# Performance work log

Hardware: AMD Instinct MI355X
Metric: run time of the kernel (lower is better)

The kernel has to match this reference:

```python
import jax, jax.numpy as jnp
import numpy as np

N, H, E, ED = 50000, 128, 600000, 32
LN_EPS = 1e-5


def _mlp(x, W1, b1, W2, b2):
    h = jax.nn.gelu(x @ W1 + b1, approximate=False)
    return h @ W2 + b2


def setup_inputs() -> dict:
    key = jax.random.key(0)
    ks = jax.random.split(key, 12)
    s = lambda fan_in: 1.0 / np.sqrt(fan_in)
    return {
        "x": jax.random.normal(ks[0], (N, H), dtype=jnp.float32),
        "edge_index": jax.random.randint(ks[1], (2, E), 0, N, dtype=jnp.int64),
        "edge_attr": jax.random.normal(ks[2], (E, ED), dtype=jnp.float32),
        "eW1": jax.random.normal(ks[3], (2 * H + ED, H), dtype=jnp.float32) * s(2 * H + ED),
        "eb1": jnp.zeros((H,), dtype=jnp.float32),
        "eW2": jax.random.normal(ks[4], (H, H), dtype=jnp.float32) * s(H),
        "eb2": jnp.zeros((H,), dtype=jnp.float32),
        "nW1": jax.random.normal(ks[5], (2 * H, H), dtype=jnp.float32) * s(2 * H),
        "nb1": jnp.zeros((H,), dtype=jnp.float32),
        "nW2": jax.random.normal(ks[6], (H, H), dtype=jnp.float32) * s(H),
        "nb2": jnp.zeros((H,), dtype=jnp.float32),
        "ln_g": jnp.ones((H,), dtype=jnp.float32),
        "ln_b": jnp.zeros((H,), dtype=jnp.float32),
    }


def reference(x, edge_index, edge_attr, eW1, eb1, eW2, eb2, nW1, nb1, nW2, nb2, ln_g, ln_b):
    src, dst = edge_index[0], edge_index[1]
    # edge MLP on gathered endpoint features + edge attrs: [E, 2H+ED] -> [E, H]
    msg = _mlp(jnp.concatenate([x[src], x[dst], edge_attr], axis=-1), eW1, eb1, eW2, eb2)
    # scatter-mean into destination nodes
    agg = jax.ops.segment_sum(msg, dst, num_segments=x.shape[0])
    count = jax.ops.segment_sum(jnp.ones((dst.shape[0], 1), dtype=x.dtype), dst, num_segments=x.shape[0])
    agg = agg / (count + 1e-8)
    # node MLP + residual + layernorm
    out = _mlp(jnp.concatenate([x, agg], axis=-1), nW1, nb1, nW2, nb2) + x
    mu = jnp.mean(out, axis=-1, keepdims=True)
    var = jnp.mean(jnp.square(out - mu), axis=-1, keepdims=True)
    return (out - mu) * jax.lax.rsqrt(var + LN_EPS) * ln_g + ln_b
```

## Files before the change

### kernel.cpp

```cpp
#include <hip/hip_runtime.h>
#include <hip/hip_fp16.h>
#include <math.h>

#define NN 50000
#define HH 128
#define EE 600000
#define EDD 32
#define NBINS 50176
#define NPRE 782

typedef __attribute__((ext_vector_type(8))) _Float16 half8;
typedef __attribute__((ext_vector_type(4))) float f32x4;

__device__ __forceinline__ unsigned pkh(float a, float b) {
  __half2 h = __floats2half2_rn(a, b);
  return *reinterpret_cast<unsigned*>(&h);
}
__device__ __forceinline__ unsigned hadd2u(unsigned a, unsigned b) {
  __half2 x = *reinterpret_cast<__half2*>(&a);
  __half2 y = *reinterpret_cast<__half2*>(&b);
  __half2 s = __hadd2(x, y);
  return *reinterpret_cast<unsigned*>(&s);
}
__device__ __forceinline__ float lo16f(unsigned u) {
  __half2 h = *reinterpret_cast<__half2*>(&u);
  return __low2float(h);
}
__device__ __forceinline__ float hi16f(unsigned u) {
  __half2 h = *reinterpret_cast<__half2*>(&u);
  return __high2float(h);
}
__device__ __forceinline__ short f2hs(float f) {
  __half h = __float2half_rn(f);
  return *reinterpret_cast<short*>(&h);
}
__device__ __forceinline__ float h2f(short s) {
  __half h = *reinterpret_cast<__half*>(&s);
  return __half2float(h);
}

__device__ __forceinline__ float gelu_f(float v) {
  float u = 2.3022082f * v * fmaf(0.044715f, v * v, 1.0f);
  float e = __builtin_amdgcn_exp2f(u);
  float r = __builtin_amdgcn_rcpf(e + 1.0f);
  return fmaf(-v, r, v);
}

#define FS 132
__global__ __launch_bounds__(256) void k_setup(
    const float* __restrict__ eW1, const float* __restrict__ nW1,
    const float* __restrict__ nW2, const float* __restrict__ eW2,
    const float* __restrict__ eb2, const long long* __restrict__ ei,
    long long nmax,
    short* __restrict__ pe1, short* __restrict__ pn1, short* __restrict__ pn2,
    short* __restrict__ pnW2p, float* __restrict__ b2p,
    int* __restrict__ zbase, int* __restrict__ flag) {
  __shared__ short sA[64 * 136];
  __shared__ float sR[64 * FS];
  __shared__ int bad;
  const int blk = blockIdx.x;
  const int tid = threadIdx.x;

  if (blk < 42) {
    const int b = blk * 4 + (tid >> 6);
    const int l = tid & 63;
    const float* W;
    short* P;
    int bb;
    if (b < 72)       { W = eW1; P = pe1; bb = b; }
    else if (b < 136) { W = nW1; P = pn1; bb = b - 72; }
    else              { W = nW2; P = pn2; bb = b - 136; }
    const int kt = bb >> 3, ct = bb & 7;
    short v[8];
#pragma unroll
    for (int j = 0; j < 8; ++j)
      v[j] = f2hs(W[(size_t)(kt * 32 + ((l >> 4) * 8 + j)) * HH + ct * 16 + (l & 15)]);
    short* dst = P + ((size_t)bb * 64 + l) * 8;
#pragma unroll
    for (int j = 0; j < 8; ++j) dst[j] = v[j];
    return;
  }
  if (blk == 42) {
    if (tid == 0) bad = 0;
    __syncthreads();
    for (int i = tid; i < 2048; i += 256) {
      long long v = ei[i];
      if (v < 0 || v >= nmax) bad = 1;
    }
    __syncthreads();
    if (tid == 0) *flag = (bad ? 0 : 1);
    return;
  }
  if (blk < 92) {
    int idx = (blk - 43) * 2048 + tid * 8;
    int4 z = {0, 0, 0, 0};
    *(int4*)(zbase + idx) = z;
    *(int4*)(zbase + idx + 4) = z;
    return;
  }
  if (blk == 94) {
    if (tid < 128) {
      float acc = 0.f;
#pragma unroll 4
      for (int k = 0; k < 128; ++k)
        acc += eb2[k] * nW1[(size_t)(128 + k) * HH + tid];
      b2p[tid] = acc;
    }
    return;
  }
  {
    const int b = blk - 92;
    const int le = tid >> 2, lq = tid & 3;
    const int wv = tid >> 6, l = tid & 63, lr = l & 15, kq = l >> 4;

    half8 bf[8];
#pragma unroll
    for (int kt = 0; kt < 4; ++kt)
#pragma unroll
      for (int c = 0; c < 2; ++c) {
        half8 v;
#pragma unroll
        for (int j = 0; j < 8; ++j)
          v[j] = (_Float16)nW1[(size_t)(128 + kt * 32 + ((l >> 4) * 8 + j)) * HH +
                               (wv * 2 + c) * 16 + (l & 15)];
        bf[kt * 2 + c] = v;
      }
    {
      const float4* xs = (const float4*)(eW2 + (size_t)(64 * b + le) * HH);
#pragma unroll
      for (int i = 0; i < 4; ++i) {
        float4 a = xs[lq * 8 + i * 2], c = xs[lq * 8 + i * 2 + 1];
        uint4 u = {pkh(a.x, a.y), pkh(a.z, a.w), pkh(c.x, c.y), pkh(c.z, c.w)};
        *(uint4*)&sA[le * 136 + lq * 32 + i * 8] = u;
      }
    }
    __syncthreads();

    f32x4 acc[4][2];
    const f32x4 zero = {0.f, 0.f, 0.f, 0.f};
#pragma unroll
    for (int m = 0; m < 4; ++m) { acc[m][0] = zero; acc[m][1] = zero; }
    const short* ab = &sA[lr * 136 + kq * 8];
#pragma unroll
    for (int kt = 0; kt < 4; ++kt) {
      half8 af[4];
#pragma unroll
      for (int m = 0; m < 4; ++m) af[m] = *(const half8*)(ab + m * 16 * 136 + kt * 32);
#pragma unroll
      for (int m = 0; m < 4; ++m)
#pragma unroll
        for (int c = 0; c < 2; ++c)
          acc[m][c] = __builtin_amdgcn_mfma_f32_16x16x32_f16(af[m], bf[kt * 2 + c], acc[m][c], 0, 0, 0);
    }
#pragma unroll
    for (int c = 0; c < 2; ++c)
#pragma unroll
      for (int m = 0; m < 4; ++m)
#pragma unroll
        for (int r = 0; r < 4; ++r)
          sR[(m * 16 + kq * 4 + r) * FS + wv * 32 + c * 16 + lr] = acc[m][c][r];
    __syncthreads();

#pragma unroll
    for (int it = 0; it < 4; ++it) {
      int item = tid + 256 * it;
      int lane = item & 63;
      int pair = item >> 6;
      int ktl = pair >> 3, ct = pair & 7;
      short v[8];
#pragma unroll
      for (int j = 0; j < 8; ++j) {
        int rowl = ktl * 32 + ((lane >> 4) * 8 + j);
        int colp = ct * 16 + (lane & 15);
        v[j] = f2hs(sR[rowl * FS + colp]);
      }
      short* dst = pnW2p + (((size_t)(2 * b + ktl) * 8 + ct) * 64 + lane) * 8;
#pragma unroll
      for (int j = 0; j < 8; ++j) dst[j] = v[j];
    }
  }
}

__global__ __launch_bounds__(256, 4) void k_preh(
    const float* __restrict__ x, const short* __restrict__ pW1,
    const void* __restrict__ eiv, const int* __restrict__ flag,
    unsigned* __restrict__ Psw, unsigned* __restrict__ Pdw,
    float* __restrict__ Hagg, int* __restrict__ chist) {
  __shared__ short sX[64 * 136];
  const int blk = blockIdx.x;
  const int tid = threadIdx.x;

  if (blk >= NPRE) {
    int e = (blk - NPRE) * 256 + tid;
    if (e < EE) {
      int d;
      if (*flag) d = (int)((const long long*)eiv)[EE + e];
      else       d = ((const int*)eiv)[EE + e];
      atomicAdd(&chist[d], 1);
    }
    return;
  }

  const int r0 = blk * 64;
  const int le = tid >> 2, lq = tid & 3;
  const int wv = tid >> 6, l = tid & 63, lr = l & 15, kq = l >> 4;

  {
    int gr = r0 + le;
    if (gr < NN) {
      float4 z = {0.f, 0.f, 0.f, 0.f};
      float4* hp = (float4*)(Hagg + (size_t)gr * HH) + lq * 8;
#pragma unroll
      for (int i = 0; i < 8; ++i) hp[i] = z;
    }
  }

  const half8* bp = (const half8*)pW1;
  half8 fa[8], fb[8];
#pragma unroll
  for (int kt = 0; kt < 4; ++kt)
#pragma unroll
    for (int c = 0; c < 2; ++c) {
      fa[kt * 2 + c] = bp[(kt * 8 + wv * 2 + c) * 64 + l];
      fb[kt * 2 + c] = bp[((kt + 4) * 8 + wv * 2 + c) * 64 + l];
    }
  {
    int gr = r0 + le;
    if (gr < NN) {
      const float4* xs = (const float4*)(x + (size_t)gr * HH);
#pragma unroll
      for (int i = 0; i < 4; ++i) {
        float4 a = xs[lq * 8 + i * 2], c = xs[lq * 8 + i * 2 + 1];
        uint4 u = {pkh(a.x, a.y), pkh(a.z, a.w), pkh(c.x, c.y), pkh(c.z, c.w)};
        *(uint4*)&sX[le * 136 + lq * 32 + i * 8] = u;
      }
    } else {
      uint4 z = {0, 0, 0, 0};
#pragma unroll
      for (int i = 0; i < 4; ++i) *(uint4*)&sX[le * 136 + lq * 32 + i * 8] = z;
    }
  }
  __syncthreads();

  f32x4 as_[4][2], ad[4][2];
  const f32x4 zero = {0.f, 0.f, 0.f, 0.f};
#pragma unroll
  for (int m = 0; m < 4; ++m) { as_[m][0] = zero; as_[m][1] = zero; ad[m][0] = zero; ad[m][1] = zero; }
  const short* ab = &sX[lr * 136 + kq * 8];
#pragma unroll
  for (int kt = 0; kt < 4; ++kt) {
    half8 af[4];
#pragma unroll
    for (int m = 0; m < 4; ++m) af[m] = *(const half8*)(ab + m * 16 * 136 + kt * 32);
#pragma unroll
    for (int m = 0; m < 4; ++m)
#pragma unroll
      for (int c = 0; c < 2; ++c) {
        as_[m][c] = __builtin_amdgcn_mfma_f32_16x16x32_f16(af[m], fa[kt * 2 + c], as_[m][c], 0, 0, 0);
        ad[m][c] = __builtin_amdgcn_mfma_f32_16x16x32_f16(af[m], fb[kt * 2 + c], ad[m][c], 0, 0, 0);
      }
  }
#pragma unroll
  for (int m = 0; m < 4; ++m)
#pragma unroll
    for (int r = 0; r < 4; ++r) {
      int grow = r0 + m * 16 + kq * 4 + r;
      if (grow < NN) {
        Psw[(size_t)grow * 64 + wv * 16 + lr] = pkh(as_[m][0][r], as_[m][1][r]);
        Pdw[(size_t)grow * 64 + wv * 16 + lr] = pkh(ad[m][0][r], ad[m][1][r]);
      }
    }
}

__global__ void k_scan1(const int* __restrict__ chist, int* __restrict__ tmp,
                        int* __restrict__ bsum) {
  __shared__ int buf[2][256];
  int t = threadIdx.x;
  int i = blockIdx.x * 256 + t;
  buf[0][t] = chist[i];
  __syncthreads();
  int cur = 0;
  for (int o = 1; o < 256; o <<= 1) {
    int v = buf[cur][t];
    if (t >= o) v += buf[cur][t - o];
    buf[cur ^ 1][t] = v;
    __syncthreads();
    cur ^= 1;
  }
  tmp[i] = buf[cur][t];
  if (t == 255) bsum[blockIdx.x] = buf[cur][255];
}

__global__ void k_scan2(int* __restrict__ bsum) {
  __shared__ int buf[2][256];
  int t = threadIdx.x;
  int orig = (t < 196) ? bsum[t] : 0;
  buf[0][t] = orig;
  __syncthreads();
  int cur = 0;
  for (int o = 1; o < 256; o <<= 1) {
    int v = buf[cur][t];
    if (t >= o) v += buf[cur][t - o];
    buf[cur ^ 1][t] = v;
    __syncthreads();
    cur ^= 1;
  }
  if (t < 196) bsum[t] = buf[cur][t] - orig;
}

__global__ void k_scatter(const void* __restrict__ eiv, const int* __restrict__ flag,
                          const int* __restrict__ tmp, const int* __restrict__ chist,
                          const int* __restrict__ bsum, int* __restrict__ cntW,
                          int4* __restrict__ e4) {
  int e = blockIdx.x * blockDim.x + threadIdx.x;
  if (e >= EE) return;
  int s, d;
  if (*flag) {
    const long long* p = (const long long*)eiv;
    s = (int)p[e];
    d = (int)p[EE + e];
  } else {
    const int* p = (const int*)eiv;
    s = p[e];
    d = p[EE + e];
  }
  int base = tmp[d] - chist[d] + bsum[d >> 8];
  int pos = base + atomicAdd(&cntW[d], 1);
  e4[pos] = make_int4(s, d, e, 0);
}

#define SFP 68
__global__ __launch_bounds__(256, 7) void k_edge(
    const unsigned* __restrict__ Psw, const unsigned* __restrict__ Pdw,
    const float* __restrict__ ea,
    const short* __restrict__ pW1, const float* __restrict__ b1,
    const int4* __restrict__ e4, float* __restrict__ Hagg) {
  __shared__ unsigned sFp[64 * SFP];
  __shared__ short sEA[64 * 40];
  __shared__ int sDst[64];

  const int tid = threadIdx.x;
  const int e0 = blockIdx.x * 64;
  const int le = tid >> 2, lq = tid & 3;
  const int wv = tid >> 6, l = tid & 63, lr = l & 15, kq = l >> 4;

  half8 w1c[2];
#pragma unroll
  for (int c = 0; c < 2; ++c)
    w1c[c] = ((const half8*)pW1)[(64 + wv * 2 + c) * 64 + l];

  const int4 er = e4[e0 + le];
  if (lq == 0) sDst[le] = er.y;

  {
    const uint4* ps = (const uint4*)(Psw + (size_t)er.x * 64);
    const uint4* pd = (const uint4*)(Pdw + (size_t)er.y * 64);
#pragma unroll
    for (int i = 0; i < 4; ++i) {
      uint4 a = ps[lq * 4 + i];
      uint4 b = pd[lq * 4 + i];
      uint4 s = {hadd2u(a.x, b.x), hadd2u(a.y, b.y), hadd2u(a.z, b.z), hadd2u(a.w, b.w)};
      *(uint4*)&sFp[le * SFP + lq * 16 + i * 4] = s;
    }
    const float4* ep = (const float4*)(ea + (size_t)er.z * EDD);
    float4 a = ep[lq * 2], b = ep[lq * 2 + 1];
    uint4 u = {pkh(a.x, a.y), pkh(a.z, a.w), pkh(b.x, b.y), pkh(b.z, b.w)};
    *(uint4*)&sEA[le * 40 + lq * 8] = u;
  }
  __syncthreads();

  f32x4 acc[4][2];
  const f32x4 zero = {0.f, 0.f, 0.f, 0.f};
#pragma unroll
  for (int m = 0; m < 4; ++m) { acc[m][0] = zero; acc[m][1] = zero; }
  {
#pragma unroll
    for (int m = 0; m < 4; ++m) {
      half8 af = *(const half8*)&sEA[(m * 16 + lr) * 40 + kq * 8];
#pragma unroll
      for (int c = 0; c < 2; ++c)
        acc[m][c] = __builtin_amdgcn_mfma_f32_16x16x32_f16(af, w1c[c], acc[m][c], 0, 0, 0);
    }
  }

  const float b1c0 = b1[wv * 32 + lr];
  const float b1c1 = b1[wv * 32 + 16 + lr];
#pragma unroll
  for (int m = 0; m < 4; ++m)
#pragma unroll
    for (int r = 0; r < 4; ++r) {
      const int row = m * 16 + kq * 4 + r;
      unsigned up = sFp[row * SFP + wv * 16 + lr];
      float v0 = acc[m][0][r] + lo16f(up) + b1c0;
      float v1 = acc[m][1][r] + hi16f(up) + b1c1;
      sFp[row * SFP + wv * 16 + lr] = pkh(gelu_f(v0), gelu_f(v1));
    }
  __syncthreads();

  {
    const int p = tid & 63;
    const int q = tid >> 6;
    const int c0 = (p >> 4) * 32 + (p & 15);
    const int rend = q * 16 + 15;
    float r0s = 0.f, r1s = 0.f;
#pragma unroll 4
    for (int r = q * 16; r <= rend; ++r) {
      unsigned u = sFp[r * SFP + p];
      r0s += lo16f(u);
      r1s += hi16f(u);
      int dcur = sDst[r];
      bool last = (r == rend) || (sDst[r + 1] != dcur);
      if (last) {
        atomicAdd(&Hagg[(size_t)dcur * HH + c0], r0s);
        atomicAdd(&Hagg[(size_t)dcur * HH + c0 + 16], r1s);
        r0s = 0.f;
        r1s = 0.f;
      }
    }
  }
}

#define NS 264
__global__ __launch_bounds__(256, 4) void k_node(
    const float* __restrict__ x,
    const float* __restrict__ Hagg, const int* __restrict__ chist,
    const short* __restrict__ pn1, const short* __restrict__ pnW2p,
    const float* __restrict__ nb1, const float* __restrict__ b2p,
    const short* __restrict__ pn2, const float* __restrict__ nb2,
    const float* __restrict__ g, const float* __restrict__ be,
    float* __restrict__ out) {
  __shared__ short sA[64 * NS];
  __shared__ float sP[64 * 4];
  __shared__ float sP2[64 * 4];
  __shared__ float sFac[64];

  const int tid = threadIdx.x;
  const int r0 = blockIdx.x * 64;
  const int le = tid >> 2;
  const int lq = tid & 3;
  const int wv = tid >> 6;
  const int l = tid & 63;
  const int lr = l & 15;
  const int kq = l >> 4;

  const half8* bpa = (const half8*)pn1;
  const half8* bpc = (const half8*)pnW2p;
  half8 b1f[16];
#pragma unroll
  for (int kt = 0; kt < 4; ++kt)
#pragma unroll
    for (int c = 0; c < 2; ++c) {
      b1f[kt * 2 + c] = bpa[(kt * 8 + wv * 2 + c) * 64 + l];
      b1f[(kt + 4) * 2 + c] = bpc[(kt * 8 + wv * 2 + c) * 64 + l];
    }

  {
    const int gr = r0 + le;
    short* row = &sA[le * NS];
    if (gr < NN) {
      float cntf = (float)chist[gr];
      float rinv = 1.0f / (cntf + 1e-8f);
      if (lq == 0) sFac[le] = cntf * rinv;
      const float4* xs = (const float4*)(x + (size_t)gr * HH);
#pragma unroll
      for (int i = 0; i < 4; ++i) {
        float4 a = xs[lq * 8 + i * 2], c = xs[lq * 8 + i * 2 + 1];
        uint4 u = {pkh(a.x, a.y), pkh(a.z, a.w), pkh(c.x, c.y), pkh(c.z, c.w)};
        *(uint4*)(row + lq * 32 + i * 8) = u;
      }
      const float4* hs = (const float4*)(Hagg + (size_t)gr * HH);
#pragma unroll
      for (int i = 0; i < 4; ++i) {
        float4 a = hs[lq * 8 + i * 2], c = hs[lq * 8 + i * 2 + 1];
        uint4 u = {pkh(a.x * rinv, a.y * rinv), pkh(a.z * rinv, a.w * rinv),
                   pkh(c.x * rinv, c.y * rinv), pkh(c.z * rinv, c.w * rinv)};
        *(uint4*)(row + 128 + lq * 32 + i * 8) = u;
      }
    } else {
      if (lq == 0) sFac[le] = 0.f;
      uint4 z = {0, 0, 0, 0};
#pragma unroll
      for (int i = 0; i < 8; ++i) *(uint4*)(row + lq * 64 + i * 8) = z;
    }
  }
  __syncthreads();

  f32x4 acc[4][2];
  const f32x4 zero = {0.f, 0.f, 0.f, 0.f};
#pragma unroll
  for (int m = 0; m < 4; ++m) { acc[m][0] = zero; acc[m][1] = zero; }
  const short* ab = &sA[lr * NS + kq * 8];
#pragma unroll
  for (int kt = 0; kt < 8; ++kt) {
    half8 af[4];
#pragma unroll
    for (int m = 0; m < 4; ++m)
      af[m] = *(const half8*)(ab + m * 16 * NS + kt * 32);
#pragma unroll
    for (int m = 0; m < 4; ++m)
#pragma unroll
      for (int c = 0; c < 2; ++c)
        acc[m][c] = __builtin_amdgcn_mfma_f32_16x16x32_f16(af[m], b1f[kt * 2 + c], acc[m][c], 0, 0, 0);
  }

  const half8* bp2 = (const half8*)pn2;
  half8 b2f_[8];
#pragma unroll
  for (int kt = 0; kt < 4; ++kt)
#pragma unroll
    for (int c = 0; c < 2; ++c)
      b2f_[kt * 2 + c] = bp2[(kt * 8 + wv * 2 + c) * 64 + l];

  __syncthreads();

#pragma unroll
  for (int c = 0; c < 2; ++c) {
    const int col = wv * 32 + c * 16 + lr;
    const float b1v = nb1[col];
    const float b2pv = b2p[col];
#pragma unroll
    for (int m = 0; m < 4; ++m)
#pragma unroll
      for (int r = 0; r < 4; ++r) {
        const int row = m * 16 + kq * 4 + r;
        float fac = sFac[row];
        sA[row * NS + 128 + col] = f2hs(gelu_f(acc[m][c][r] + b1v + fac * b2pv));
      }
  }
  __syncthreads();

  f32x4 acc2[4][2];
#pragma unroll
  for (int m = 0; m < 4; ++m) { acc2[m][0] = zero; acc2[m][1] = zero; }
#pragma unroll
  for (int kt = 0; kt < 4; ++kt) {
    half8 af[4];
#pragma unroll
    for (int m = 0; m < 4; ++m)
      af[m] = *(const half8*)(ab + m * 16 * NS + 128 + kt * 32);
#pragma unroll
    for (int m = 0; m < 4; ++m)
#pragma unroll
      for (int c = 0; c < 2; ++c)
        acc2[m][c] = __builtin_amdgcn_mfma_f32_16x16x32_f16(af[m], b2f_[kt * 2 + c], acc2[m][c], 0, 0, 0);
  }

  float val[4][2][4];
#pragma unroll
  for (int c = 0; c < 2; ++c) {
    const int col = wv * 32 + c * 16 + lr;
    const float b2v = nb2[col];
#pragma unroll
    for (int m = 0; m < 4; ++m)
#pragma unroll
      for (int r = 0; r < 4; ++r) {
        const int lrow = m * 16 + kq * 4 + r;
        float xr = h2f(sA[lrow * NS + col]);
        val[m][c][r] = acc2[m][c][r] + b2v + xr;
      }
  }
#pragma unroll
  for (int m = 0; m < 4; ++m)
#pragma unroll
    for (int r = 0; r < 4; ++r) {
      float s = val[m][0][r] + val[m][1][r];
      float s2 = val[m][0][r] * val[m][0][r] + val[m][1][r] * val[m][1][r];
#pragma unroll
      for (int o = 1; o < 16; o <<= 1) {
        s += __shfl_xor(s, o);
        s2 += __shfl_xor(s2, o);
      }
      if (lr == 0) {
        const int row = m * 16 + kq * 4 + r;
        sP[row * 4 + wv] = s;
        sP2[row * 4 + wv] = s2;
      }
    }
  __syncthreads();

#pragma unroll
  for (int c = 0; c < 2; ++c) {
    const int col = wv * 32 + c * 16 + lr;
    const float gv = g[col];
    const float bv = be[col];
#pragma unroll
    for (int m = 0; m < 4; ++m)
#pragma unroll
      for (int r = 0; r < 4; ++r) {
        const int lrow = m * 16 + kq * 4 + r;
        const int row = r0 + lrow;
        if (row < NN) {
          float4 ps = *(float4*)&sP[lrow * 4];
          float4 qs = *(float4*)&sP2[lrow * 4];
          float s = ps.x + ps.y + ps.z + ps.w;
          float s2 = qs.x + qs.y + qs.z + qs.w;
          float mu = s * 0.0078125f;
          float var = s2 * 0.0078125f - mu * mu;
          float rs = rsqrtf(var + 1e-5f);
          out[(size_t)row * HH + col] = (val[m][c][r] - mu) * rs * gv + bv;
        }
      }
  }
}

extern "C" void kernel_launch(void* const* d_in, const int* in_sizes, int n_in,
                              void* d_out, int out_size, void* d_ws, size_t ws_size,
                              hipStream_t stream) {
  const float* x = (const float*)d_in[0];
  const void* ei = d_in[1];
  const float* ea = (const float*)d_in[2];
  const float* eW1 = (const float*)d_in[3];
  const float* eb1 = (const float*)d_in[4];
  const float* eW2 = (const float*)d_in[5];
  const float* eb2 = (const float*)d_in[6];
  const float* nW1 = (const float*)d_in[7];
  const float* nb1 = (const float*)d_in[8];
  const float* nW2 = (const float*)d_in[9];
  const float* nb2 = (const float*)d_in[10];
  const float* lng = (const float*)d_in[11];
  const float* lnb = (const float*)d_in[12];
  float* out = (float*)d_out;

  char* w = (char*)d_ws;
  size_t off = 0;
  auto alloc = [&](size_t bytes) { void* p = w + off; off = (off + bytes + 255) & ~(size_t)255; return p; };
  float* Hagg = (float*)alloc((size_t)NN * HH * 4);
  int* chist = (int*)alloc((size_t)NBINS * 4);
  int* cntW = (int*)alloc((size_t)NBINS * 4);
  short* pe1 = (short*)alloc((size_t)72 * 512 * 2);
  short* pn1 = (short*)alloc((size_t)64 * 512 * 2);
  short* pn2 = (short*)alloc((size_t)32 * 512 * 2);
  short* pnW2p = (short*)alloc((size_t)32 * 512 * 2);
  float* b2p = (float*)alloc(HH * 4);
  int4* e4 = (int4*)alloc((size_t)EE * 16);
  int* tmpS = (int*)alloc((size_t)NBINS * 4);
  int* bsum = (int*)alloc(256 * 4);
  int* flag = (int*)alloc(256);
  unsigned* Psw = (unsigned*)alloc((size_t)NN * 64 * 4);
  unsigned* Pdw = (unsigned*)alloc((size_t)NN * 64 * 4);

  k_setup<<<95, 256, 0, stream>>>(eW1, nW1, nW2, eW2, eb2, (const long long*)ei,
                                  (long long)NN, pe1, pn1, pn2, pnW2p, b2p, chist, flag);
  k_preh<<<NPRE + (EE + 255) / 256, 256, 0, stream>>>(x, pe1, ei, flag, Psw, Pdw, Hagg, chist);
  k_scan1<<<NBINS / 256, 256, 0, stream>>>(chist, tmpS, bsum);
  k_scan2<<<1, 256, 0, stream>>>(bsum);
  k_scatter<<<(EE + 255) / 256, 256, 0, stream>>>(ei, flag, tmpS, chist, bsum, cntW, e4);
  k_edge<<<EE / 64, 256, 0, stream>>>(Psw, Pdw, ea, pe1, eb1, e4, Hagg);
  k_node<<<(NN + 63) / 64, 256, 0, stream>>>(x, Hagg, chist, pn1, pnW2p, nb1, b2p, pn2, nb2, lng, lnb, out);
}
```

Before: 170.9 us.

## Accumulate aggregation in packed fp16, pack edge records, fuse scan, swizzle edge blocks

The per-node aggregation buffer changes from fp32 to packed half2 and is updated with half2 atomic adds, halving atomic traffic and the node kernel's read bandwidth. Edge records shrink from int4 to a packed 64-bit word, the second scan is folded into the scatter kernel to drop a launch, and edge workgroups are remapped across XCDs so sorted neighbouring destinations stay in one L2. The edge kernel's output tile is transposed in shared memory for vectorised reads, with the nW2 packing permuted to match. Accumulating sums in fp16 risks precision loss or overflow for high-degree nodes.

```diff
diff --git a/kernel.cpp b/kernel.cpp
--- a/kernel.cpp
+++ b/kernel.cpp
@@ -8,6 +8,7 @@
 #define EDD 32
 #define NBINS 50176
 #define NPRE 782
+#define NWG_E (EE / 64)
 
 typedef __attribute__((ext_vector_type(8))) _Float16 half8;
 typedef __attribute__((ext_vector_type(4))) float f32x4;
@@ -20,6 +21,12 @@
   __half2 x = *reinterpret_cast<__half2*>(&a);
   __half2 y = *reinterpret_cast<__half2*>(&b);
   __half2 s = __hadd2(x, y);
+  return *reinterpret_cast<unsigned*>(&s);
+}
+__device__ __forceinline__ unsigned hmul2u(unsigned a, unsigned b) {
+  __half2 x = *reinterpret_cast<__half2*>(&a);
+  __half2 y = *reinterpret_cast<__half2*>(&b);
+  __half2 s = __hmul2(x, y);
   return *reinterpret_cast<unsigned*>(&s);
 }
 __device__ __forceinline__ float lo16f(unsigned u) {
@@ -170,7 +177,9 @@
       short v[8];
 #pragma unroll
       for (int j = 0; j < 8; ++j) {
-        int rowl = ktl * 32 + ((lane >> 4) * 8 + j);
+        int kpos = ktl * 32 + ((lane >> 4) * 8 + j);
+        int t2 = kpos >> 1, h2 = kpos & 1;
+        int rowl = (t2 >> 4) * 32 + (t2 & 15) + 16 * h2;
         int colp = ct * 16 + (lane & 15);
         v[j] = f2hs(sR[rowl * FS + colp]);
       }
@@ -185,7 +194,7 @@
     const float* __restrict__ x, const short* __restrict__ pW1,
     const void* __restrict__ eiv, const int* __restrict__ flag,
     unsigned* __restrict__ Psw, unsigned* __restrict__ Pdw,
-    float* __restrict__ Hagg, int* __restrict__ chist) {
+    unsigned* __restrict__ HaggH2, int* __restrict__ chist) {
   __shared__ short sX[64 * 136];
   const int blk = blockIdx.x;
   const int tid = threadIdx.x;
@@ -208,10 +217,10 @@
   {
     int gr = r0 + le;
     if (gr < NN) {
-      float4 z = {0.f, 0.f, 0.f, 0.f};
-      float4* hp = (float4*)(Hagg + (size_t)gr * HH) + lq * 8;
-#pragma unroll
-      for (int i = 0; i < 8; ++i) hp[i] = z;
+      uint4 z = {0, 0, 0, 0};
+      uint4* hp = (uint4*)(HaggH2 + (size_t)gr * 64);
+#pragma unroll
+      for (int i = 0; i < 4; ++i) hp[lq * 4 + i] = z;
     }
   }
 
@@ -291,28 +300,27 @@
   if (t == 255) bsum[blockIdx.x] = buf[cur][255];
 }
 
-__global__ void k_scan2(int* __restrict__ bsum) {
-  __shared__ int buf[2][256];
-  int t = threadIdx.x;
-  int orig = (t < 196) ? bsum[t] : 0;
-  buf[0][t] = orig;
-  __syncthreads();
-  int cur = 0;
-  for (int o = 1; o < 256; o <<= 1) {
-    int v = buf[cur][t];
-    if (t >= o) v += buf[cur][t - o];
-    buf[cur ^ 1][t] = v;
-    __syncthreads();
-    cur ^= 1;
-  }
-  if (t < 196) bsum[t] = buf[cur][t] - orig;
-}
-
 __global__ void k_scatter(const void* __restrict__ eiv, const int* __restrict__ flag,
                           const int* __restrict__ tmp, const int* __restrict__ chist,
                           const int* __restrict__ bsum, int* __restrict__ cntW,
-                          int4* __restrict__ e4) {
-  int e = blockIdx.x * blockDim.x + threadIdx.x;
+                          unsigned long long* __restrict__ e8) {
+  __shared__ int sB[2][256];
+  const int t = threadIdx.x;
+  int orig = (t < 196) ? bsum[t] : 0;
+  sB[0][t] = orig;
+  __syncthreads();
+  int cur = 0;
+  for (int o = 1; o < 256; o <<= 1) {
+    int v = sB[cur][t];
+    if (t >= o) v += sB[cur][t - o];
+    sB[cur ^ 1][t] = v;
+    __syncthreads();
+    cur ^= 1;
+  }
+  sB[1][t] = sB[0][t] - orig;
+  __syncthreads();
+
+  int e = blockIdx.x * 256 + t;
   if (e >= EE) return;
   int s, d;
   if (*flag) {
@@ -324,9 +332,10 @@
     s = p[e];
     d = p[EE + e];
   }
-  int base = tmp[d] - chist[d] + bsum[d >> 8];
+  int base = tmp[d] - chist[d] + sB[1][d >> 8];
   int pos = base + atomicAdd(&cntW[d], 1);
-  e4[pos] = make_int4(s, d, e, 0);
+  e8[pos] = (unsigned long long)s | ((unsigned long long)d << 20) |
+            ((unsigned long long)e << 40);
 }
 
 #define SFP 68
@@ -334,13 +343,19 @@
     const unsigned* __restrict__ Psw, const unsigned* __restrict__ Pdw,
     const float* __restrict__ ea,
     const short* __restrict__ pW1, const float* __restrict__ b1,
-    const int4* __restrict__ e4, float* __restrict__ Hagg) {
+    const unsigned long long* __restrict__ e8, unsigned* __restrict__ HaggH2) {
   __shared__ unsigned sFp[64 * SFP];
   __shared__ short sEA[64 * 40];
   __shared__ int sDst[64];
 
+  int orig = blockIdx.x;
+  const int q8 = NWG_E >> 3, r8 = NWG_E & 7;
+  int xcd = orig & 7, lid = orig >> 3;
+  int swz = (xcd < r8) ? xcd * (q8 + 1) + lid
+                       : r8 * (q8 + 1) + (xcd - r8) * q8 + lid;
+
   const int tid = threadIdx.x;
-  const int e0 = blockIdx.x * 64;
+  const int e0 = swz * 64;
   const int le = tid >> 2, lq = tid & 3;
   const int wv = tid >> 6, l = tid & 63, lr = l & 15, kq = l >> 4;
 
@@ -349,12 +364,15 @@
   for (int c = 0; c < 2; ++c)
     w1c[c] = ((const half8*)pW1)[(64 + wv * 2 + c) * 64 + l];
 
-  const int4 er = e4[e0 + le];
-  if (lq == 0) sDst[le] = er.y;
-
-  {
-    const uint4* ps = (const uint4*)(Psw + (size_t)er.x * 64);
-    const uint4* pd = (const uint4*)(Pdw + (size_t)er.y * 64);
+  const unsigned long long er = e8[e0 + le];
+  const int gs = (int)(er & 0xFFFFF);
+  const int gd = (int)((er >> 20) & 0xFFFFF);
+  const int ge = (int)(er >> 40);
+  if (lq == 0) sDst[le] = gd;
+
+  {
+    const uint4* ps = (const uint4*)(Psw + (size_t)gs * 64);
+    const uint4* pd = (const uint4*)(Pdw + (size_t)gd * 64);
 #pragma unroll
     for (int i = 0; i < 4; ++i) {
       uint4 a = ps[lq * 4 + i];
@@ -362,7 +380,7 @@
       uint4 s = {hadd2u(a.x, b.x), hadd2u(a.y, b.y), hadd2u(a.z, b.z), hadd2u(a.w, b.w)};
       *(uint4*)&sFp[le * SFP + lq * 16 + i * 4] = s;
     }
-    const float4* ep = (const float4*)(ea + (size_t)er.z * EDD);
+    const float4* ep = (const float4*)(ea + (size_t)ge * EDD);
     float4 a = ep[lq * 2], b = ep[lq * 2 + 1];
     uint4 u = {pkh(a.x, a.y), pkh(a.z, a.w), pkh(b.x, b.y), pkh(b.z, b.w)};
     *(uint4*)&sEA[le * 40 + lq * 8] = u;
@@ -385,6 +403,7 @@
 
   const float b1c0 = b1[wv * 32 + lr];
   const float b1c1 = b1[wv * 32 + 16 + lr];
+  unsigned pr[4][4];
 #pragma unroll
   for (int m = 0; m < 4; ++m)
 #pragma unroll
@@ -393,28 +412,43 @@
       unsigned up = sFp[row * SFP + wv * 16 + lr];
       float v0 = acc[m][0][r] + lo16f(up) + b1c0;
       float v1 = acc[m][1][r] + hi16f(up) + b1c1;
-      sFp[row * SFP + wv * 16 + lr] = pkh(gelu_f(v0), gelu_f(v1));
-    }
+      pr[m][r] = pkh(gelu_f(v0), gelu_f(v1));
+    }
+  __syncthreads();
+
+  {
+    unsigned* tp = &sFp[(wv * 16 + lr) * SFP];
+#pragma unroll
+    for (int m = 0; m < 4; ++m) {
+      uint4 u = {pr[m][0], pr[m][1], pr[m][2], pr[m][3]};
+      *(uint4*)&tp[m * 16 + kq * 4] = u;
+    }
+  }
   __syncthreads();
 
   {
     const int p = tid & 63;
     const int q = tid >> 6;
-    const int c0 = (p >> 4) * 32 + (p & 15);
+    const unsigned* tp2 = &sFp[p * SFP + q * 16];
     const int rend = q * 16 + 15;
     float r0s = 0.f, r1s = 0.f;
-#pragma unroll 4
-    for (int r = q * 16; r <= rend; ++r) {
-      unsigned u = sFp[r * SFP + p];
-      r0s += lo16f(u);
-      r1s += hi16f(u);
-      int dcur = sDst[r];
-      bool last = (r == rend) || (sDst[r + 1] != dcur);
-      if (last) {
-        atomicAdd(&Hagg[(size_t)dcur * HH + c0], r0s);
-        atomicAdd(&Hagg[(size_t)dcur * HH + c0 + 16], r1s);
-        r0s = 0.f;
-        r1s = 0.f;
+#pragma unroll
+    for (int i = 0; i < 4; ++i) {
+      uint4 u4 = *(const uint4*)&tp2[i * 4];
+      unsigned uu[4] = {u4.x, u4.y, u4.z, u4.w};
+#pragma unroll
+      for (int j = 0; j < 4; ++j) {
+        int r = q * 16 + i * 4 + j;
+        r0s += lo16f(uu[j]);
+        r1s += hi16f(uu[j]);
+        int dcur = sDst[r];
+        bool last = (r == rend) || (sDst[r + 1] != dcur);
+        if (last) {
+          unsafeAtomicAdd((__half2*)&HaggH2[(size_t)dcur * 64 + p],
+                          __floats2half2_rn(r0s, r1s));
+          r0s = 0.f;
+          r1s = 0.f;
+        }
       }
     }
   }
@@ -423,7 +457,7 @@
 #define NS 264
 __global__ __launch_bounds__(256, 4) void k_node(
     const float* __restrict__ x,
-    const float* __restrict__ Hagg, const int* __restrict__ chist,
+    const unsigned* __restrict__ HaggH2, const int* __restrict__ chist,
     const short* __restrict__ pn1, const short* __restrict__ pnW2p,
     const float* __restrict__ nb1, const float* __restrict__ b2p,
     const short* __restrict__ pn2, const float* __restrict__ nb2,
@@ -468,12 +502,15 @@
         uint4 u = {pkh(a.x, a.y), pkh(a.z, a.w), pkh(c.x, c.y), pkh(c.z, c.w)};
         *(uint4*)(row + lq * 32 + i * 8) = u;
       }
-      const float4* hs = (const float4*)(Hagg + (size_t)gr * HH);
+      const unsigned rv2 = pkh(rinv, rinv);
+      const uint4* hs = (const uint4*)(HaggH2 + (size_t)gr * 64);
 #pragma unroll
       for (int i = 0; i < 4; ++i) {
-        float4 a = hs[lq * 8 + i * 2], c = hs[lq * 8 + i * 2 + 1];
-        uint4 u = {pkh(a.x * rinv, a.y * rinv), pkh(a.z * rinv, a.w * rinv),
-                   pkh(c.x * rinv, c.y * rinv), pkh(c.z * rinv, c.w * rinv)};
+        uint4 u = hs[lq * 4 + i];
+        u.x = hmul2u(u.x, rv2);
+        u.y = hmul2u(u.y, rv2);
+        u.z = hmul2u(u.z, rv2);
+        u.w = hmul2u(u.w, rv2);
         *(uint4*)(row + 128 + lq * 32 + i * 8) = u;
       }
     } else {
@@ -624,7 +661,7 @@
   char* w = (char*)d_ws;
   size_t off = 0;
   auto alloc = [&](size_t bytes) { void* p = w + off; off = (off + bytes + 255) & ~(size_t)255; return p; };
-  float* Hagg = (float*)alloc((size_t)NN * HH * 4);
+  unsigned* HaggH2 = (unsigned*)alloc((size_t)NN * 64 * 4);
   int* chist = (int*)alloc((size_t)NBINS * 4);
   int* cntW = (int*)alloc((size_t)NBINS * 4);
   short* pe1 = (short*)alloc((size_t)72 * 512 * 2);
@@ -632,7 +669,7 @@
   short* pn2 = (short*)alloc((size_t)32 * 512 * 2);
   short* pnW2p = (short*)alloc((size_t)32 * 512 * 2);
   float* b2p = (float*)alloc(HH * 4);
-  int4* e4 = (int4*)alloc((size_t)EE * 16);
+  unsigned long long* e8 = (unsigned long long*)alloc((size_t)EE * 8);
   int* tmpS = (int*)alloc((size_t)NBINS * 4);
   int* bsum = (int*)alloc(256 * 4);
   int* flag = (int*)alloc(256);
@@ -641,10 +678,9 @@
 
   k_setup<<<95, 256, 0, stream>>>(eW1, nW1, nW2, eW2, eb2, (const long long*)ei,
                                   (long long)NN, pe1, pn1, pn2, pnW2p, b2p, chist, flag);
-  k_preh<<<NPRE + (EE + 255) / 256, 256, 0, stream>>>(x, pe1, ei, flag, Psw, Pdw, Hagg, chist);
+  k_preh<<<NPRE + (EE + 255) / 256, 256, 0, stream>>>(x, pe1, ei, flag, Psw, Pdw, HaggH2, chist);
   k_scan1<<<NBINS / 256, 256, 0, stream>>>(chist, tmpS, bsum);
-  k_scan2<<<1, 256, 0, stream>>>(bsum);
-  k_scatter<<<(EE + 255) / 256, 256, 0, stream>>>(ei, flag, tmpS, chist, bsum, cntW, e4);
-  k_edge<<<EE / 64, 256, 0, stream>>>(Psw, Pdw, ea, pe1, eb1, e4, Hagg);
-  k_node<<<(NN + 63) / 64, 256, 0, stream>>>(x, Hagg, chist, pn1, pnW2p, nb1, b2p, pn2, nb2, lng, lnb, out);
-}
+  k_scatter<<<(EE + 255) / 256, 256, 0, stream>>>(ei, flag, tmpS, chist, bsum, cntW, e8);
+  k_edge<<<NWG_E, 256, 0, stream>>>(Psw, Pdw, ea, pe1, eb1, e8, HaggH2);
+  k_node<<<(NN + 63) / 64, 256, 0, stream>>>(x, HaggH2, chist, pn1, pnW2p, nb1, b2p, pn2, nb2, lng, lnb, out);
+}
```

Measured after the change: 156.4 us. 8.5% less time.
